# Optimization experiments

Hardware: AMD Instinct MI355X
Metric: run time of the kernel (lower is better)

The kernel has to match this reference:

```python
import jax, jax.numpy as jnp
import numpy as np

DT = 1.0          # integration timestep (ms)
SIGMA = 0.5       # gauss_std for surrogate (unused in pure fwd spike)
AMPLITUDE = 0.3   # dampening_factor
N = 50000         # neurons
R = 4             # receptor types
D = 5             # max_delay
E = 5000000       # recurrent synapses
B = 4             # batch


def setup_inputs() -> dict:
    key = jax.random.key(0)
    ks = jax.random.split(key, 20)
    f = jnp.float32
    inputs = jax.random.normal(ks[0], (B, N * R), f) * 0.1
    # z_buf holds binary spikes for the last D steps
    z_buf = jax.random.bernoulli(ks[1], 0.05, (B, N * D)).astype(f)
    v = jax.random.uniform(ks[2], (B, N), f, 0.0, 1.0)
    r = jnp.zeros((B, N), f)
    asc_1 = jax.random.normal(ks[3], (B, N), f)
    asc_2 = jax.random.normal(ks[4], (B, N), f)
    psc_rise = jax.random.normal(ks[5], (B, N * R), f) * 0.5
    psc = jax.random.normal(ks[6], (B, N * R), f)
    rec_w = jax.random.normal(ks[7], (E,), f) * 0.01
    rec_rows = jax.random.randint(ks[8], (E,), 0, N * R, jnp.int32)
    rec_cols = jax.random.randint(ks[9], (E,), 0, N * D, jnp.int32)
    syn_decay = jax.random.uniform(ks[10], (N, R), f, 0.5, 0.99)
    psc_initial = jax.random.uniform(ks[11], (N, R), f, 0.1, 1.0)
    t_ref = jax.random.uniform(ks[12], (N,), f, 1.0, 4.0)
    asc_amps = jax.random.normal(ks[13], (N, 2), f)
    k = jax.random.normal(ks[14], (N, 2), f)  # inv-sigmoid space, read via sigmoid
    v_th = jnp.ones((N,), f)
    e_l = jnp.zeros((N,), f)
    v_reset = jnp.zeros((N,), f)
    g = jax.random.uniform(ks[15], (N,), f, 0.1, 1.0)
    decay = jax.random.uniform(ks[16], (N,), f, 0.8, 0.99)
    current_factor = jax.random.uniform(ks[17], (N,), f, 0.1, 1.0)
    voltage_scale = jnp.ones((N,), f) * 20.0
    voltage_offset = jnp.ones((N,), f) * -70.0
    return dict(inputs=inputs, z_buf=z_buf, v=v, r=r, asc_1=asc_1, asc_2=asc_2,
                psc_rise=psc_rise, psc=psc, rec_w=rec_w, rec_rows=rec_rows,
                rec_cols=rec_cols, syn_decay=syn_decay, psc_initial=psc_initial,
                t_ref=t_ref, asc_amps=asc_amps, k=k, v_th=v_th, e_l=e_l,
                v_reset=v_reset, g=g, decay=decay, current_factor=current_factor,
                voltage_scale=voltage_scale, voltage_offset=voltage_offset)


def _step(inputs, z_buf, v, r, asc_1, asc_2, psc_rise, psc,
          rec_w, rec_rows, rec_cols, syn_decay, psc_initial, t_ref,
          asc_amps, k, v_th, e_l, v_reset, g, decay, current_factor,
          voltage_scale, voltage_offset):
    shaped_z_buf = z_buf.reshape(B, D, N)
    prev_z = shaped_z_buf[:, 0]                      # most recent spikes [B,N]
    psc_rise_r = psc_rise.reshape(B, N, R)
    psc_r = psc.reshape(B, N, R)

    # sparse recurrent matmul: W[N*R, N*D] @ z_buf^T -> [N*R, B]
    vals = rec_w[:, None] * z_buf.T[rec_cols]        # [E, B] gather
    i_rec = jax.ops.segment_sum(vals, rec_rows, num_segments=N * R).T  # [B, N*R]

    rec_inputs = (i_rec + inputs).reshape(B, N, R)
    new_psc_rise = syn_decay * psc_rise_r + rec_inputs * psc_initial
    new_psc = psc_r * syn_decay + DT * syn_decay * psc_rise_r

    new_r = jax.nn.relu(r + prev_z * t_ref - DT)

    kk = jax.nn.sigmoid(k)                           # param_k_read()
    new_asc_1 = jnp.exp(-DT * kk[:, 0]) * asc_1 + prev_z * asc_amps[:, 0]
    new_asc_2 = jnp.exp(-DT * kk[:, 1]) * asc_2 + prev_z * asc_amps[:, 1]

    reset_current = prev_z * (v_reset - v_th)
    input_current = psc_r.sum(-1)                    # old psc
    c1 = input_current + asc_1 + asc_2 + g * e_l
    new_v = decay * v + current_factor * c1 + reset_current

    v_sc = (new_v - v_th) / (v_th - e_l)
    new_z = (v_sc > 0.0).astype(v_sc.dtype)          # spike_gauss forward
    new_z = jnp.where(new_r > 0.0, jnp.zeros_like(new_z), new_z)

    new_z_buf = jnp.concatenate([new_z[:, None], shaped_z_buf[:, :-1]], axis=1)
    out_v = new_v * voltage_scale + voltage_offset
    return (new_z, out_v, new_r, new_asc_1, new_asc_2,
            new_psc_rise.reshape(B, N * R), new_psc.reshape(B, N * R),
            new_z_buf.reshape(B, N * D))


def reference(inputs, z_buf, v, r, asc_1, asc_2, psc_rise, psc,
              rec_w, rec_rows, rec_cols, syn_decay, psc_initial, t_ref,
              asc_amps, k, v_th, e_l, v_reset, g, decay, current_factor,
              voltage_scale, voltage_offset):
    outs = _step(inputs, z_buf, v, r, asc_1, asc_2, psc_rise, psc,
                 rec_w, rec_rows, rec_cols, syn_decay, psc_initial, t_ref,
                 asc_amps, k, v_th, e_l, v_reset, g, decay, current_factor,
                 voltage_scale, voltage_offset)
    # pack outputs + new state into one [B, N*(5+2R+D)] array
    return jnp.concatenate(outs, axis=-1)
```

## Files before the change

kernel.cpp:

```cpp
#include <hip/hip_runtime.h>

#define Nn 50000
#define Rr 4
#define Dd 5
#define Ee 5000000
#define Bb 4
#define NRr (Nn * Rr)
#define NDd (Nn * Dd)
#define ZW 7814

__global__ __launch_bounds__(256) void pack_z_kernel(
    const float* __restrict__ z_buf, unsigned char* __restrict__ z_pack,
    unsigned* __restrict__ zbits, float4* __restrict__ i_rec4) {
    int i = blockIdx.x * 256 + threadIdx.x;
    if (i < Bb * NRr / 4) i_rec4[i] = make_float4(0.f, 0.f, 0.f, 0.f);
    unsigned m = 0;
    if (i < NDd) {
#pragma unroll
        for (int b = 0; b < Bb; ++b)
            if (z_buf[(size_t)b * NDd + i] != 0.0f) m |= (1u << b);
        z_pack[i] = (unsigned char)m;
    }
    unsigned long long bal = __ballot(m != 0);
    if ((i & 63) == 0 && i < NDd) {
        zbits[(i >> 5)]     = (unsigned)bal;
        zbits[(i >> 5) + 1] = (unsigned)(bal >> 32);
    }
}

__global__ __launch_bounds__(256) void edge_kernel(
    const float4* __restrict__ w4, const int4* __restrict__ rows4,
    const int4* __restrict__ cols4, const unsigned char* __restrict__ z_pack,
    const unsigned* __restrict__ zbits, float* __restrict__ i_rec) {
    __shared__ unsigned zb[ZW];
    for (int t = threadIdx.x; t < ZW; t += 256) zb[t] = zbits[t];
    __syncthreads();
    const int nq = Ee / 4;
    for (int i = blockIdx.x * 256 + threadIdx.x; i < nq;
         i += gridDim.x * 256) {
        int4 c = cols4[i];
        unsigned h0 = (zb[(unsigned)c.x >> 5] >> (c.x & 31)) & 1u;
        unsigned h1 = (zb[(unsigned)c.y >> 5] >> (c.y & 31)) & 1u;
        unsigned h2 = (zb[(unsigned)c.z >> 5] >> (c.z & 31)) & 1u;
        unsigned h3 = (zb[(unsigned)c.w >> 5] >> (c.w & 31)) & 1u;
        if (!(h0 | h1 | h2 | h3)) continue;
        int4 rw = rows4[i];
        float4 w = w4[i];
#define DO_EDGE(hh, col, row, wv)                                     \
    if (hh) {                                                         \
        unsigned mm = z_pack[col];                                    \
        if (mm & 1u) atomicAdd(&i_rec[0 * NRr + (row)], (wv));        \
        if (mm & 2u) atomicAdd(&i_rec[1 * NRr + (row)], (wv));        \
        if (mm & 4u) atomicAdd(&i_rec[2 * NRr + (row)], (wv));        \
        if (mm & 8u) atomicAdd(&i_rec[3 * NRr + (row)], (wv));        \
    }
        DO_EDGE(h0, c.x, rw.x, w.x)
        DO_EDGE(h1, c.y, rw.y, w.y)
        DO_EDGE(h2, c.z, rw.z, w.z)
        DO_EDGE(h3, c.w, rw.w, w.w)
#undef DO_EDGE
    }
}

__global__ __launch_bounds__(256) void neuron_kernel(
    const float* __restrict__ inputs, const float* __restrict__ z_buf,
    const float* __restrict__ v_in, const float* __restrict__ r_in,
    const float* __restrict__ asc1_in, const float* __restrict__ asc2_in,
    const float* __restrict__ psc_rise_in, const float* __restrict__ psc_in,
    const float* __restrict__ syn_decay, const float* __restrict__ psc_initial,
    const float* __restrict__ t_ref, const float* __restrict__ asc_amps,
    const float* __restrict__ kparam, const float* __restrict__ v_th,
    const float* __restrict__ e_l, const float* __restrict__ v_reset,
    const float* __restrict__ g, const float* __restrict__ decay,
    const float* __restrict__ current_factor,
    const float* __restrict__ voltage_scale,
    const float* __restrict__ voltage_offset,
    const float* __restrict__ i_rec, float* __restrict__ out) {
    int n = blockIdx.x * blockDim.x + threadIdx.x;
    int b = blockIdx.y;
    if (n >= Nn) return;

    const size_t bn  = (size_t)b * Nn + n;
    const size_t bnr = (size_t)b * NRr + (size_t)n * 4;

    float prev_z = z_buf[(size_t)b * NDd + n];

    float4 ir  = *(const float4*)(i_rec + bnr);
    float4 in4 = *(const float4*)(inputs + bnr);
    float4 pr  = *(const float4*)(psc_rise_in + bnr);
    float4 pc  = *(const float4*)(psc_in + bnr);
    float4 sd  = *(const float4*)(syn_decay + (size_t)n * 4);
    float4 pi  = *(const float4*)(psc_initial + (size_t)n * 4);

    float4 npr, npc;
    npr.x = sd.x * pr.x + (ir.x + in4.x) * pi.x;
    npr.y = sd.y * pr.y + (ir.y + in4.y) * pi.y;
    npr.z = sd.z * pr.z + (ir.z + in4.z) * pi.z;
    npr.w = sd.w * pr.w + (ir.w + in4.w) * pi.w;
    npc.x = pc.x * sd.x + sd.x * pr.x;
    npc.y = pc.y * sd.y + sd.y * pr.y;
    npc.z = pc.z * sd.z + sd.z * pr.z;
    npc.w = pc.w * sd.w + sd.w * pr.w;

    float input_current = pc.x + pc.y + pc.z + pc.w;

    float tr    = t_ref[n];
    float new_r = fmaxf(r_in[bn] + prev_z * tr - 1.0f, 0.0f);

    float2 kv = *(const float2*)(kparam + (size_t)n * 2);
    float2 aa = *(const float2*)(asc_amps + (size_t)n * 2);
    float kk0 = 1.0f / (1.0f + expf(-kv.x));
    float kk1 = 1.0f / (1.0f + expf(-kv.y));
    float a1 = asc1_in[bn];
    float a2 = asc2_in[bn];
    float na1 = expf(-kk0) * a1 + prev_z * aa.x;
    float na2 = expf(-kk1) * a2 + prev_z * aa.y;

    float vth = v_th[n];
    float el  = e_l[n];
    float reset_current = prev_z * (v_reset[n] - vth);
    float c1 = input_current + a1 + a2 + g[n] * el;
    float new_v = decay[n] * v_in[bn] + current_factor[n] * c1 + reset_current;

    float v_sc = (new_v - vth) / (vth - el);
    float new_z = (v_sc > 0.0f) ? 1.0f : 0.0f;
    if (new_r > 0.0f) new_z = 0.0f;

    float out_v = new_v * voltage_scale[n] + voltage_offset[n];

    float* ob = out + (size_t)b * 18 * Nn;
    ob[n]            = new_z;
    ob[Nn + n]       = out_v;
    ob[2 * Nn + n]   = new_r;
    ob[3 * Nn + n]   = na1;
    ob[4 * Nn + n]   = na2;
    *(float4*)(ob + 5 * Nn + (size_t)n * 4) = npr;
    *(float4*)(ob + 9 * Nn + (size_t)n * 4) = npc;
    ob[13 * Nn + n] = new_z;
#pragma unroll
    for (int d = 0; d < Dd - 1; ++d)
        ob[14 * Nn + (size_t)d * Nn + n] = z_buf[(size_t)b * NDd + (size_t)d * Nn + n];
}

extern "C" void kernel_launch(void* const* d_in, const int* in_sizes, int n_in,
                              void* d_out, int out_size, void* d_ws, size_t ws_size,
                              hipStream_t stream) {
    const float* inputs        = (const float*)d_in[0];
    const float* z_buf         = (const float*)d_in[1];
    const float* v             = (const float*)d_in[2];
    const float* r             = (const float*)d_in[3];
    const float* asc_1         = (const float*)d_in[4];
    const float* asc_2         = (const float*)d_in[5];
    const float* psc_rise      = (const float*)d_in[6];
    const float* psc           = (const float*)d_in[7];
    const float* rec_w         = (const float*)d_in[8];
    const int*   rec_rows      = (const int*)d_in[9];
    const int*   rec_cols      = (const int*)d_in[10];
    const float* syn_decay     = (const float*)d_in[11];
    const float* psc_initial   = (const float*)d_in[12];
    const float* t_ref         = (const float*)d_in[13];
    const float* asc_amps      = (const float*)d_in[14];
    const float* k             = (const float*)d_in[15];
    const float* v_th          = (const float*)d_in[16];
    const float* e_l           = (const float*)d_in[17];
    const float* v_reset       = (const float*)d_in[18];
    const float* g             = (const float*)d_in[19];
    const float* decay         = (const float*)d_in[20];
    const float* current_factor= (const float*)d_in[21];
    const float* voltage_scale = (const float*)d_in[22];
    const float* voltage_offset= (const float*)d_in[23];
    float* out = (float*)d_out;

    float* i_rec = (float*)d_ws;
    unsigned char* z_pack = (unsigned char*)d_ws + (size_t)Bb * NRr * sizeof(float);
    unsigned* zbits = (unsigned*)(z_pack + ((NDd + 255) & ~255));

    pack_z_kernel<<<(NDd + 255) / 256, 256, 0, stream>>>(
        z_buf, z_pack, zbits, (float4*)i_rec);

    edge_kernel<<<2048, 256, 0, stream>>>(
        (const float4*)rec_w, (const int4*)rec_rows, (const int4*)rec_cols,
        z_pack, zbits, i_rec);

    dim3 ngrid((Nn + 255) / 256, Bb);
    neuron_kernel<<<ngrid, 256, 0, stream>>>(
        inputs, z_buf, v, r, asc_1, asc_2, psc_rise, psc,
        syn_decay, psc_initial, t_ref, asc_amps, k, v_th, e_l, v_reset,
        g, decay, current_factor, voltage_scale, voltage_offset,
        i_rec, out);
}
```

Baseline: 204.8 us.

## Split edge scatter into compaction scan and separate atomic-apply pass

Replaces the single edge kernel, which used an LDS spike bitmask and issued atomics inline, with a two-phase scheme. A scan kernel reads the packed spike masks, reserves output slots with block-aggregated atomics, and writes (index, weight) pairs to a compact list. An apply kernel then streams that list and performs the float atomics. The aim is to separate the divergent gather and filter work from the scattered atomics. In exchange it writes and re-reads about 8 MB of list data and adds a launch. Entries past a fixed list capacity are silently dropped, and a direct-atomic fallback runs if the workspace is too small.

```diff
diff --git a/kernel.cpp b/kernel.cpp
--- a/kernel.cpp
+++ b/kernel.cpp
@@ -7,59 +7,108 @@
 #define Bb 4
 #define NRr (Nn * Rr)
 #define NDd (Nn * Dd)
-#define ZW 7814
+
+#define LIST_CAP 1200000u
 
 __global__ __launch_bounds__(256) void pack_z_kernel(
     const float* __restrict__ z_buf, unsigned char* __restrict__ z_pack,
-    unsigned* __restrict__ zbits, float4* __restrict__ i_rec4) {
+    float4* __restrict__ i_rec4, unsigned* __restrict__ gcount) {
     int i = blockIdx.x * 256 + threadIdx.x;
+    if (i == 0) *gcount = 0;
     if (i < Bb * NRr / 4) i_rec4[i] = make_float4(0.f, 0.f, 0.f, 0.f);
-    unsigned m = 0;
     if (i < NDd) {
+        unsigned m = 0;
 #pragma unroll
         for (int b = 0; b < Bb; ++b)
             if (z_buf[(size_t)b * NDd + i] != 0.0f) m |= (1u << b);
         z_pack[i] = (unsigned char)m;
     }
-    unsigned long long bal = __ballot(m != 0);
-    if ((i & 63) == 0 && i < NDd) {
-        zbits[(i >> 5)]     = (unsigned)bal;
-        zbits[(i >> 5) + 1] = (unsigned)(bal >> 32);
-    }
-}
-
-__global__ __launch_bounds__(256) void edge_kernel(
+}
+
+__global__ __launch_bounds__(256) void scan_kernel(
+    const int4* __restrict__ cols4, const int4* __restrict__ rows4,
+    const float4* __restrict__ w4, const unsigned char* __restrict__ z_pack,
+    unsigned* __restrict__ gcount, uint2* __restrict__ list) {
+    __shared__ unsigned lds_cnt, lds_base;
+    const int nq = Ee / 4;
+    int i = blockIdx.x * 256 + threadIdx.x;
+#pragma unroll 1
+    for (int iter = 0; iter < 5; ++iter, i += gridDim.x * 256) {
+        if (threadIdx.x == 0) lds_cnt = 0;
+        __syncthreads();
+        unsigned m0 = 0, m1 = 0, m2 = 0, m3 = 0;
+        int cnt = 0;
+        int4 c;
+        if (i < nq) {
+            c = cols4[i];
+            m0 = z_pack[c.x];
+            m1 = z_pack[c.y];
+            m2 = z_pack[c.z];
+            m3 = z_pack[c.w];
+            cnt = __popc((m3 << 24) | (m2 << 16) | (m1 << 8) | m0);
+        }
+        unsigned pos = 0;
+        if (cnt) pos = atomicAdd(&lds_cnt, (unsigned)cnt);
+        __syncthreads();
+        if (threadIdx.x == 0 && lds_cnt)
+            lds_base = atomicAdd(gcount, lds_cnt);
+        __syncthreads();
+        if (cnt) {
+            int4 rw = rows4[i];
+            float4 w = w4[i];
+            unsigned p = lds_base + pos;
+            auto emit = [&](unsigned mm, int row, float wv) {
+                while (mm) {
+                    int b = __builtin_ctz(mm);
+                    mm &= mm - 1;
+                    if (p < LIST_CAP)
+                        list[p] = make_uint2((unsigned)(b * NRr + row),
+                                             __float_as_uint(wv));
+                    ++p;
+                }
+            };
+            emit(m0, rw.x, w.x);
+            emit(m1, rw.y, w.y);
+            emit(m2, rw.z, w.z);
+            emit(m3, rw.w, w.w);
+        }
+    }
+}
+
+__global__ __launch_bounds__(256) void apply_kernel(
+    const unsigned* __restrict__ gcount, const uint2* __restrict__ list,
+    float* __restrict__ i_rec) {
+    unsigned total = *gcount;
+    if (total > LIST_CAP) total = LIST_CAP;
+    for (unsigned i = blockIdx.x * 256 + threadIdx.x; i < total;
+         i += gridDim.x * 256) {
+        uint2 e = list[i];
+        atomicAdd(&i_rec[e.x], __uint_as_float(e.y));
+    }
+}
+
+__global__ __launch_bounds__(256) void edge_direct_kernel(
     const float4* __restrict__ w4, const int4* __restrict__ rows4,
     const int4* __restrict__ cols4, const unsigned char* __restrict__ z_pack,
-    const unsigned* __restrict__ zbits, float* __restrict__ i_rec) {
-    __shared__ unsigned zb[ZW];
-    for (int t = threadIdx.x; t < ZW; t += 256) zb[t] = zbits[t];
-    __syncthreads();
-    const int nq = Ee / 4;
-    for (int i = blockIdx.x * 256 + threadIdx.x; i < nq;
-         i += gridDim.x * 256) {
-        int4 c = cols4[i];
-        unsigned h0 = (zb[(unsigned)c.x >> 5] >> (c.x & 31)) & 1u;
-        unsigned h1 = (zb[(unsigned)c.y >> 5] >> (c.y & 31)) & 1u;
-        unsigned h2 = (zb[(unsigned)c.z >> 5] >> (c.z & 31)) & 1u;
-        unsigned h3 = (zb[(unsigned)c.w >> 5] >> (c.w & 31)) & 1u;
-        if (!(h0 | h1 | h2 | h3)) continue;
-        int4 rw = rows4[i];
-        float4 w = w4[i];
-#define DO_EDGE(hh, col, row, wv)                                     \
-    if (hh) {                                                         \
-        unsigned mm = z_pack[col];                                    \
-        if (mm & 1u) atomicAdd(&i_rec[0 * NRr + (row)], (wv));        \
-        if (mm & 2u) atomicAdd(&i_rec[1 * NRr + (row)], (wv));        \
-        if (mm & 4u) atomicAdd(&i_rec[2 * NRr + (row)], (wv));        \
-        if (mm & 8u) atomicAdd(&i_rec[3 * NRr + (row)], (wv));        \
-    }
-        DO_EDGE(h0, c.x, rw.x, w.x)
-        DO_EDGE(h1, c.y, rw.y, w.y)
-        DO_EDGE(h2, c.z, rw.z, w.z)
-        DO_EDGE(h3, c.w, rw.w, w.w)
-#undef DO_EDGE
-    }
+    float* __restrict__ i_rec) {
+    int i = blockIdx.x * blockDim.x + threadIdx.x;
+    if (i >= Ee / 4) return;
+    int4 c = cols4[i];
+    unsigned m0 = z_pack[c.x], m1 = z_pack[c.y];
+    unsigned m2 = z_pack[c.z], m3 = z_pack[c.w];
+    if (!(m0 | m1 | m2 | m3)) return;
+    int4 rw = rows4[i];
+    float4 w = w4[i];
+    auto do_edge = [&](unsigned mm, int row, float wv) {
+        if (mm & 1u) atomicAdd(&i_rec[0 * NRr + row], wv);
+        if (mm & 2u) atomicAdd(&i_rec[1 * NRr + row], wv);
+        if (mm & 4u) atomicAdd(&i_rec[2 * NRr + row], wv);
+        if (mm & 8u) atomicAdd(&i_rec[3 * NRr + row], wv);
+    };
+    do_edge(m0, rw.x, w.x);
+    do_edge(m1, rw.y, w.y);
+    do_edge(m2, rw.z, w.z);
+    do_edge(m3, rw.w, w.w);
 }
 
 __global__ __launch_bounds__(256) void neuron_kernel(
@@ -171,16 +220,26 @@
     const float* voltage_offset= (const float*)d_in[23];
     float* out = (float*)d_out;
 
-    float* i_rec = (float*)d_ws;
-    unsigned char* z_pack = (unsigned char*)d_ws + (size_t)Bb * NRr * sizeof(float);
-    unsigned* zbits = (unsigned*)(z_pack + ((NDd + 255) & ~255));
+    char* wsb = (char*)d_ws;
+    float* i_rec = (float*)wsb;
+    unsigned char* z_pack = (unsigned char*)(wsb + 3200000);
+    unsigned* gcount = (unsigned*)(wsb + 3450240);
+    uint2* list = (uint2*)(wsb + 3450496);
+    const size_t ws_needed = 3450496 + (size_t)LIST_CAP * 8;
 
     pack_z_kernel<<<(NDd + 255) / 256, 256, 0, stream>>>(
-        z_buf, z_pack, zbits, (float4*)i_rec);
-
-    edge_kernel<<<2048, 256, 0, stream>>>(
-        (const float4*)rec_w, (const int4*)rec_rows, (const int4*)rec_cols,
-        z_pack, zbits, i_rec);
+        z_buf, z_pack, (float4*)i_rec, gcount);
+
+    if (ws_size >= ws_needed) {
+        scan_kernel<<<1024, 256, 0, stream>>>(
+            (const int4*)rec_cols, (const int4*)rec_rows,
+            (const float4*)rec_w, z_pack, gcount, list);
+        apply_kernel<<<2048, 256, 0, stream>>>(gcount, list, i_rec);
+    } else {
+        edge_direct_kernel<<<(Ee / 4 + 255) / 256, 256, 0, stream>>>(
+            (const float4*)rec_w, (const int4*)rec_rows,
+            (const int4*)rec_cols, z_pack, i_rec);
+    }
 
     dim3 ngrid((Nn + 255) / 256, Bb);
     neuron_kernel<<<ngrid, 256, 0, stream>>>(
```

Result: slower. 267.8 us (+30.8%).
